# Performance work log

Hardware: AMD Instinct MI355X
Metric: run time of the kernel (lower is better)

Reference implementation:

```python
import jax, jax.numpy as jnp
import numpy as np

TEMPERATURE = 1.0

def setup_inputs() -> dict:
    key = jax.random.key(0)
    k1, k2 = jax.random.split(key)
    N = 16384
    velocities = jax.random.normal(k1, (N, 3), dtype=jnp.float32)
    positions = jax.random.normal(k2, (N, 3), dtype=jnp.float32)
    return {"velocities": velocities, "positions": positions}

def reference(velocities, positions):
    # positions are unused by the original module's forward math
    norm = jnp.linalg.norm(velocities, axis=-1, keepdims=True)
    vel_norm = velocities / (norm + 1e-6)                      # (N, 3)
    similarity = vel_norm @ vel_norm.T                          # (N, N)
    affinity = jnp.exp(similarity / TEMPERATURE)                # (N, N)
    assignments = affinity / jnp.sum(affinity, axis=1, keepdims=True)
    entropy = -jnp.sum(assignments * jnp.log(assignments + 1e-8), axis=1)
    return jnp.mean(entropy)
```

## Files before the change

### kernel.cpp

```cpp
#include <hip/hip_runtime.h>
#include <math.h>

#define TPB 256
#define DEG 10
#define NMON 286
#define PCH 16


__global__ __launch_bounds__(TPB) void prep_kernel(const float* __restrict__ vel,
                                                   float4* __restrict__ U,
                                                   float* __restrict__ CT,
                                                   float* __restrict__ out, int N) {
    int i = blockIdx.x * TPB + threadIdx.x;
    if (i < NMON) CT[i] = 0.0f;
    if (i == NMON) out[0] = 0.0f;
    if (i < N) {
        float x = vel[3 * i], y = vel[3 * i + 1], z = vel[3 * i + 2];
        float n = sqrtf(fmaf(x, x, fmaf(y, y, z * z))) + 1e-6f;
        float r = 1.0f / n;
        U[i] = make_float4(x * r, y * r, z * r, 0.0f);
    }
}

__global__ __launch_bounds__(TPB) void moments_kernel(const float4* __restrict__ U,
                                                      float* __restrict__ CT, int N) {
    int mon = blockIdx.x;
    int rem = mon, aa = 0, bb = 0;
    for (;; ++aa) {
        int R = DEG - aa, cnt = (R + 1) * (R + 2) / 2;
        if (rem < cnt) break;
        rem -= cnt;
    }
    for (;; ++bb) {
        int cnt = DEG - aa - bb + 1;
        if (rem < cnt) break;
        rem -= cnt;
    }
    int cc = rem;

    int base = blockIdx.y * (N / PCH);
    float acc = 0.0f;
#pragma unroll
    for (int q = 0; q < (N / PCH) / TPB; ++q) {
        int j = base + q * TPB + threadIdx.x;
        float4 u = U[j];
        float x = u.x, y = u.y, z = u.z;
        float x2 = x * x, x4 = x2 * x2, x8 = x4 * x4;
        float y2 = y * y, y4 = y2 * y2, y8 = y4 * y4;
        float z2 = z * z, z4 = z2 * z2, z8 = z4 * z4;
        float m = 1.0f;
        m *= (aa & 1) ? x : 1.0f;  m *= (aa & 2) ? x2 : 1.0f;
        m *= (aa & 4) ? x4 : 1.0f; m *= (aa & 8) ? x8 : 1.0f;
        m *= (bb & 1) ? y : 1.0f;  m *= (bb & 2) ? y2 : 1.0f;
        m *= (bb & 4) ? y4 : 1.0f; m *= (bb & 8) ? y8 : 1.0f;
        m *= (cc & 1) ? z : 1.0f;  m *= (cc & 2) ? z2 : 1.0f;
        m *= (cc & 4) ? z4 : 1.0f; m *= (cc & 8) ? z8 : 1.0f;
        acc += m;
    }

    for (int off = 32; off; off >>= 1) acc += __shfl_down(acc, off);
    __shared__ float red[TPB / 64];
    if ((threadIdx.x & 63) == 0) red[threadIdx.x >> 6] = acc;
    __syncthreads();
    if (threadIdx.x == 0) {
        float Msum = 0.0f;
        for (int w = 0; w < TPB / 64; ++w) Msum += red[w];
        float f = 1.0f;
        for (int q = 2; q <= aa; ++q) f *= (float)q;
        for (int q = 2; q <= bb; ++q) f *= (float)q;
        for (int q = 2; q <= cc; ++q) f *= (float)q;
        atomicAdd(&CT[mon], Msum / f);
    }
}

__global__ __launch_bounds__(TPB) void rows_kernel(const float4* __restrict__ U,
                                                   const float* __restrict__ CT,
                                                   float* __restrict__ out, int N) {
    __shared__ float ct[NMON];
    int tid = threadIdx.x;
    for (int k = tid; k < NMON; k += TPB) ct[k] = CT[k];
    __syncthreads();

    int i = blockIdx.x * TPB + tid;
    float contrib = 0.0f;
    if (i < N) {
        float4 u = U[i];
        float x = u.x, y = u.y, z = u.z;

        float Z = 0.f, S = 0.f;
        int idx = 0;
        float xa = 1.f;
        for (int a = 0; a <= DEG; ++a) {
            float yb = 1.f;
            for (int b = 0; b <= DEG - a; ++b) {
                float xy = xa * yb;
                float abf = (float)(a + b);
                float zc = 1.f, cf = 0.f;
                for (int c = 0; c <= DEG - a - b; ++c) {
                    float p = xy * zc * ct[idx];
                    Z += p;
                    S = fmaf(abf + cf, p, S);
                    zc *= z;
                    cf += 1.0f;
                    ++idx;
                }
                yb *= y;
            }
            xa *= x;
        }
        float H = logf(Z) - S / Z - 1e-8f * (float)N;
        contrib = H / (float)N;
    }
    for (int off = 32; off; off >>= 1) contrib += __shfl_down(contrib, off);
    __shared__ float red[TPB / 64];
    if ((threadIdx.x & 63) == 0) red[threadIdx.x >> 6] = contrib;
    __syncthreads();
    if (threadIdx.x == 0) {
        float s = 0.f;
        for (int w = 0; w < TPB / 64; ++w) s += red[w];
        atomicAdd(out, s);
    }
}

extern "C" void kernel_launch(void* const* d_in, const int* in_sizes, int n_in,
                              void* d_out, int out_size, void* d_ws, size_t ws_size,
                              hipStream_t stream) {
    const float* vel = (const float*)d_in[0];
    int N = in_sizes[0] / 3;
    float* out = (float*)d_out;

    char* ws = (char*)d_ws;
    float4* U = (float4*)ws;
    float* CT = (float*)(ws + (size_t)N * sizeof(float4));

    int nb = (N + TPB - 1) / TPB;
    prep_kernel<<<nb, TPB, 0, stream>>>(vel, U, CT, out, N);
    dim3 mg(NMON, PCH);
    moments_kernel<<<mg, TPB, 0, stream>>>(U, CT, N);
    rows_kernel<<<nb, TPB, 0, stream>>>(U, CT, out, N);
}
```

Baseline: 68.57 us.

## Fuse normalization into moment and row kernels, replace atomics with partial buffers

Removes the separate prep kernel by recomputing the velocity normalization inside both the moments and rows kernels. Per-chunk moment partials and per-block row sums are written to buffers instead of accumulated with atomics. A small finalize kernel and a device-to-device copy then produce the output. This trades one launch and the atomic contention for redundant normalization math, an extra launch plus a memcpy, and strided 3-float loads.

```diff
diff --git a/kernel.cpp b/kernel.cpp
--- a/kernel.cpp
+++ b/kernel.cpp
@@ -7,24 +7,10 @@
 #define PCH 16
 
 
-__global__ __launch_bounds__(TPB) void prep_kernel(const float* __restrict__ vel,
-                                                   float4* __restrict__ U,
-                                                   float* __restrict__ CT,
-                                                   float* __restrict__ out, int N) {
-    int i = blockIdx.x * TPB + threadIdx.x;
-    if (i < NMON) CT[i] = 0.0f;
-    if (i == NMON) out[0] = 0.0f;
-    if (i < N) {
-        float x = vel[3 * i], y = vel[3 * i + 1], z = vel[3 * i + 2];
-        float n = sqrtf(fmaf(x, x, fmaf(y, y, z * z))) + 1e-6f;
-        float r = 1.0f / n;
-        U[i] = make_float4(x * r, y * r, z * r, 0.0f);
-    }
-}
+__global__ __launch_bounds__(TPB) void moments_kernel(const float* __restrict__ vel,
+                                                      float* __restrict__ CTp, int N) {
+    int mon = blockIdx.x;
 
-__global__ __launch_bounds__(TPB) void moments_kernel(const float4* __restrict__ U,
-                                                      float* __restrict__ CT, int N) {
-    int mon = blockIdx.x;
     int rem = mon, aa = 0, bb = 0;
     for (;; ++aa) {
         int R = DEG - aa, cnt = (R + 1) * (R + 2) / 2;
@@ -43,8 +29,10 @@
 #pragma unroll
     for (int q = 0; q < (N / PCH) / TPB; ++q) {
         int j = base + q * TPB + threadIdx.x;
-        float4 u = U[j];
-        float x = u.x, y = u.y, z = u.z;
+        float x = vel[3 * j], y = vel[3 * j + 1], z = vel[3 * j + 2];
+        float n = sqrtf(fmaf(x, x, fmaf(y, y, z * z))) + 1e-6f;
+        float r = 1.0f / n;
+        x *= r; y *= r; z *= r;
         float x2 = x * x, x4 = x2 * x2, x8 = x4 * x4;
         float y2 = y * y, y4 = y2 * y2, y8 = y4 * y4;
         float z2 = z * z, z4 = z2 * z2, z8 = z4 * z4;
@@ -69,23 +57,30 @@
         for (int q = 2; q <= aa; ++q) f *= (float)q;
         for (int q = 2; q <= bb; ++q) f *= (float)q;
         for (int q = 2; q <= cc; ++q) f *= (float)q;
-        atomicAdd(&CT[mon], Msum / f);
+        CTp[(size_t)blockIdx.y * NMON + mon] = Msum / f;
     }
 }
 
-__global__ __launch_bounds__(TPB) void rows_kernel(const float4* __restrict__ U,
-                                                   const float* __restrict__ CT,
-                                                   float* __restrict__ out, int N) {
+__global__ __launch_bounds__(TPB) void rows_kernel(const float* __restrict__ vel,
+                                                   const float* __restrict__ CTp,
+                                                   float* __restrict__ rowpart, int N) {
     __shared__ float ct[NMON];
     int tid = threadIdx.x;
-    for (int k = tid; k < NMON; k += TPB) ct[k] = CT[k];
+    for (int k = tid; k < NMON; k += TPB) {
+        float s = 0.0f;
+#pragma unroll
+        for (int ch = 0; ch < PCH; ++ch) s += CTp[(size_t)ch * NMON + k];
+        ct[k] = s;
+    }
     __syncthreads();
 
     int i = blockIdx.x * TPB + tid;
     float contrib = 0.0f;
     if (i < N) {
-        float4 u = U[i];
-        float x = u.x, y = u.y, z = u.z;
+        float x = vel[3 * i], y = vel[3 * i + 1], z = vel[3 * i + 2];
+        float n = sqrtf(fmaf(x, x, fmaf(y, y, z * z))) + 1e-6f;
+        float r = 1.0f / n;
+        x *= r; y *= r; z *= r;
 
         float Z = 0.f, S = 0.f;
         int idx = 0;
@@ -113,13 +108,22 @@
     }
     for (int off = 32; off; off >>= 1) contrib += __shfl_down(contrib, off);
     __shared__ float red[TPB / 64];
-    if ((threadIdx.x & 63) == 0) red[threadIdx.x >> 6] = contrib;
+    if ((tid & 63) == 0) red[tid >> 6] = contrib;
     __syncthreads();
-    if (threadIdx.x == 0) {
+    if (tid == 0) {
         float s = 0.f;
         for (int w = 0; w < TPB / 64; ++w) s += red[w];
-        atomicAdd(out, s);
+        rowpart[blockIdx.x] = s;
     }
+}
+
+__global__ void finalize_kernel(const float* __restrict__ rowpart,
+                                float* __restrict__ result, int nb) {
+    float s = 0.0f;
+    int lane = threadIdx.x;
+    for (int k = lane; k < nb; k += 64) s += rowpart[k];
+    for (int off = 32; off; off >>= 1) s += __shfl_down(s, off);
+    if (lane == 0) result[0] = s;
 }
 
 extern "C" void kernel_launch(void* const* d_in, const int* in_sizes, int n_in,
@@ -127,15 +131,15 @@
                               hipStream_t stream) {
     const float* vel = (const float*)d_in[0];
     int N = in_sizes[0] / 3;
-    float* out = (float*)d_out;
 
-    char* ws = (char*)d_ws;
-    float4* U = (float4*)ws;
-    float* CT = (float*)(ws + (size_t)N * sizeof(float4));
+    float* CTp = (float*)d_ws;
+    float* rowpart = CTp + PCH * NMON;
+    float* result = rowpart + 64;
 
     int nb = (N + TPB - 1) / TPB;
-    prep_kernel<<<nb, TPB, 0, stream>>>(vel, U, CT, out, N);
     dim3 mg(NMON, PCH);
-    moments_kernel<<<mg, TPB, 0, stream>>>(U, CT, N);
-    rows_kernel<<<nb, TPB, 0, stream>>>(U, CT, out, N);
+    moments_kernel<<<mg, TPB, 0, stream>>>(vel, CTp, N);
+    rows_kernel<<<nb, TPB, 0, stream>>>(vel, CTp, rowpart, N);
+    finalize_kernel<<<1, 64, 0, stream>>>(rowpart, result, nb);
+    hipMemcpyAsync(d_out, result, sizeof(float), hipMemcpyDeviceToDevice, stream);
 }
```

Result: slower. 72.45 us (+5.7%).
